# Kernel tuning notes

Hardware: AMD Instinct MI355X
Metric: run time of the kernel (lower is better)

The kernel has to match this reference:

```python
import jax, jax.numpy as jnp
import numpy as np

N_NODES = 100_000
N_EDGES = 3_200_000
F_IN, F_HID, F_OUT = 128, 128, 128
MLP_HID, MLP_OUT = 256, 64


def setup_inputs() -> dict:
    key = jax.random.key(0)
    ks = jax.random.split(key, 11)
    def w(k, shape):
        fan_in = shape[0]
        return jax.random.normal(k, shape, jnp.float32) / jnp.sqrt(jnp.float32(fan_in))
    return {
        'x':   jax.random.normal(ks[0], (N_NODES, F_IN), jnp.float32),
        'src': jax.random.randint(ks[1], (N_EDGES,), 0, N_NODES, jnp.int32),
        'dst': jax.random.randint(ks[2], (N_EDGES,), 0, N_NODES, jnp.int32),
        'w1':  w(ks[3], (F_IN, F_HID)),  'b1': jnp.zeros((F_HID,), jnp.float32),
        'w2':  w(ks[4], (F_HID, F_OUT)), 'b2': jnp.zeros((F_OUT,), jnp.float32),
        'wm1': w(ks[5], (F_OUT, MLP_HID)), 'bm1': jnp.zeros((MLP_HID,), jnp.float32),
        'wm2': w(ks[6], (MLP_HID, MLP_OUT)), 'bm2': jnp.zeros((MLP_OUT,), jnp.float32),
    }


def reference(x, src, dst, w1, b1, w2, b2, wm1, bm1, wm2, bm2):
    n = x.shape[0]
    ones = jnp.ones(src.shape[0], x.dtype)
    # DGL GraphConv norm='both': clamp degrees to >=1, symmetric D^-1/2 A D^-1/2
    out_norm = jnp.clip(jax.ops.segment_sum(ones, src, num_segments=n), 1.0) ** -0.5
    in_norm = jnp.clip(jax.ops.segment_sum(ones, dst, num_segments=n), 1.0) ** -0.5

    def gconv(h, w, b):
        msg = (h * out_norm[:, None])[src]                       # [E, F] gather
        agg = jax.ops.segment_sum(msg, dst, num_segments=n)      # [N, F] scatter-add
        return (agg * in_norm[:, None]) @ w + b

    h = jax.nn.relu(gconv(x, w1, b1))   # conv1 + relu (dropout is identity in eval)
    h = jax.nn.relu(gconv(h, w2, b2))   # conv2 + relu
    h = jax.nn.relu(h @ wm1 + bm1)      # MLP hidden layer
    return h @ wm2 + bm2                # MLP output (no final activation)
```

## Files before the change

### kernel.cpp

```cpp
#include <hip/hip_runtime.h>
#include <hip/hip_bf16.h>
#include <cstdint>

__device__ __forceinline__ unsigned short f2b(float f) {
    union { float f; unsigned int i; } v; v.f = f;
    unsigned int i = v.i;
    unsigned int r = (i + 0x7FFFu + ((i >> 16) & 1u)) >> 16;
    return (unsigned short)r;
}
__device__ __forceinline__ float b2f_lo(unsigned int p) {
    union { unsigned int i; float f; } v; v.i = p << 16; return v.f;
}
__device__ __forceinline__ float b2f_hi(unsigned int p) {
    union { unsigned int i; float f; } v; v.i = p & 0xFFFF0000u; return v.f;
}
__device__ __forceinline__ unsigned int pack2(float a, float b) {
    return (unsigned int)f2b(a) | ((unsigned int)f2b(b) << 16);
}

typedef __attribute__((__ext_vector_type__(8))) __bf16 bf16x8;
typedef __attribute__((__ext_vector_type__(4))) float  f32x4;

#define N_NODES 100000
#define N_EDGES 3200000
#define NBUCK   400
#define BSZ     250
#define NCHUNK  256
#define CHUNK   12500
#define BCAP    9216

__global__ void k_hist2(const int* __restrict__ src, const int* __restrict__ dst,
                        int* __restrict__ gcntA, int* __restrict__ gcntB,
                        int* __restrict__ blkA, int* __restrict__ blkB, int E) {
    __shared__ int hA[NBUCK], hB[NBUCK];
    int t = threadIdx.x, b = blockIdx.x;
    int lo = b * CHUNK, hi = min(lo + CHUNK, E);
    for (int j = t; j < NBUCK; j += 256) { hA[j] = 0; hB[j] = 0; }
    __syncthreads();
    for (int i = lo + t; i < hi; i += 256) {
        atomicAdd(&hA[dst[i] / BSZ], 1);
        atomicAdd(&hB[src[i] / BSZ], 1);
    }
    __syncthreads();
    for (int j = t; j < NBUCK; j += 256) {
        blkA[b * NBUCK + j] = hA[j];
        blkB[b * NBUCK + j] = hB[j];
        if (hA[j]) atomicAdd(&gcntA[j], hA[j]);
        if (hB[j]) atomicAdd(&gcntB[j], hB[j]);
    }
}

__global__ void k_scan_coarse(const int* __restrict__ gcntA, const int* __restrict__ gcntB,
                              int* __restrict__ gbaseA, int* __restrict__ gbaseB,
                              int* __restrict__ gcurA, int* __restrict__ gcurB,
                              int* __restrict__ offsets) {
    __shared__ int pA[512], pB[512];
    int t = threadIdx.x;
    int vA = (t < NBUCK) ? gcntA[t] : 0;
    int vB = (t < NBUCK) ? gcntB[t] : 0;
    pA[t] = vA; pB[t] = vB;
    __syncthreads();
    for (int d = 1; d < 512; d <<= 1) {
        int a = (t >= d) ? pA[t - d] : 0;
        int b = (t >= d) ? pB[t - d] : 0;
        __syncthreads();
        pA[t] += a; pB[t] += b;
        __syncthreads();
    }
    if (t < NBUCK) {
        gbaseA[t] = pA[t] - vA; gcurA[t] = pA[t] - vA;
        gbaseB[t] = pB[t] - vB; gcurB[t] = pB[t] - vB;
    }
    if (t == 511) {
        gbaseA[NBUCK] = pA[511];
        gbaseB[NBUCK] = pB[511];
        offsets[N_NODES] = pA[511];
    }
}

__global__ void k_scatter(const int* __restrict__ src, const int* __restrict__ dst,
                          int* __restrict__ gcurA, int* __restrict__ gcurB,
                          const int* __restrict__ blkA, const int* __restrict__ blkB,
                          unsigned* __restrict__ pairs, unsigned short* __restrict__ keysB,
                          int E) {
    __shared__ int baA[NBUCK], baB[NBUCK], lcA[NBUCK], lcB[NBUCK];
    int t = threadIdx.x, b = blockIdx.x;
    int lo = b * CHUNK, hi = min(lo + CHUNK, E);
    for (int j = t; j < NBUCK; j += 256) {
        int hA = blkA[b * NBUCK + j];
        baA[j] = hA ? atomicAdd(&gcurA[j], hA) : 0;
        lcA[j] = 0;
        int hB = blkB[b * NBUCK + j];
        baB[j] = hB ? atomicAdd(&gcurB[j], hB) : 0;
        lcB[j] = 0;
    }
    __syncthreads();
    for (int i = lo + t; i < hi; i += 256) {
        int s = src[i], d = dst[i];
        int bA = d / BSZ;
        int l  = atomicAdd(&lcA[bA], 1);
        pairs[baA[bA] + l] = ((unsigned)(d - bA * BSZ) << 17) | (unsigned)s;
        int bB = s / BSZ;
        int l2 = atomicAdd(&lcB[bB], 1);
        keysB[baB[bB] + l2] = (unsigned short)(s - bB * BSZ);
    }
}

__global__ __launch_bounds__(512)
void k_csr_sort(const unsigned* __restrict__ pairs, const int* __restrict__ gbaseA,
                int* __restrict__ offsets, float* __restrict__ in_norm,
                int* __restrict__ esrc) {
    __shared__ int el[BCAP];
    __shared__ int hist[256], scan[256], curs[256];
    int b = blockIdx.x, t = threadIdx.x;
    int node0 = b * BSZ;
    int bstart = gbaseA[b], bend = gbaseA[b + 1];
    int cnt = bend - bstart;
    if (t < 256) hist[t] = 0;
    __syncthreads();
    for (int i = bstart + t; i < bend; i += 512)
        atomicAdd(&hist[pairs[i] >> 17], 1);
    __syncthreads();
    if (t < 256) scan[t] = hist[t];
    __syncthreads();
    for (int d = 1; d < 256; d <<= 1) {
        int v = (t < 256 && t >= d) ? scan[t - d] : 0;
        __syncthreads();
        if (t < 256) scan[t] += v;
        __syncthreads();
    }
    if (t < BSZ) {
        int excl = scan[t] - hist[t];
        offsets[node0 + t] = bstart + excl;
        in_norm[node0 + t] = rsqrtf((float)max(hist[t], 1));
        curs[t] = excl;
    }
    __syncthreads();
    for (int i = bstart + t; i < bend; i += 512) {
        unsigned p = pairs[i];
        int d = (int)(p >> 17);
        int l = atomicAdd(&curs[d], 1);
        el[l] = (int)(p & 0x1FFFFu);
    }
    __syncthreads();
    int wv = t >> 6, lane = t & 63;
    const int INF = 0x7FFFFFFF;
    for (int n = wv; n < BSZ; n += 8) {
        int len = hist[n];
        if (len <= 1) continue;
        int base = scan[n] - len;
        if (len <= 64) {
            int v0 = (lane < len) ? el[base + lane] : INF;
#pragma unroll
            for (int k = 2; k <= 64; k <<= 1) {
#pragma unroll
                for (int d = 32; d > 0; d >>= 1) {
                    if (d >= k) continue;
                    int w0 = __shfl_xor(v0, d, 64);
                    bool up = ((lane & k) == 0);
                    bool lower = ((lane & d) == 0);
                    v0 = (lower == up) ? min(v0, w0) : max(v0, w0);
                }
            }
            if (lane < len) el[base + lane] = v0;
        } else {
            int v0 = (lane < len) ? el[base + lane] : INF;
            int v1 = (64 + lane < len) ? el[base + 64 + lane] : INF;
#pragma unroll
            for (int k = 2; k <= 128; k <<= 1) {
#pragma unroll
                for (int d = 64; d > 0; d >>= 1) {
                    if (d >= k) continue;
                    if (d == 64) {
                        int a = min(v0, v1), bb = max(v0, v1);
                        v0 = a; v1 = bb;
                    } else {
                        int w0 = __shfl_xor(v0, d, 64);
                        int w1 = __shfl_xor(v1, d, 64);
                        bool up0 = ((lane & k) == 0);
                        bool up1 = (((64 + lane) & k) == 0);
                        bool lower = ((lane & d) == 0);
                        v0 = (lower == up0) ? min(v0, w0) : max(v0, w0);
                        v1 = (lower == up1) ? min(v1, w1) : max(v1, w1);
                    }
                }
            }
            if (lane < len) el[base + lane] = v0;
            if (64 + lane < len) el[base + 64 + lane] = v1;
        }
    }
    __syncthreads();
    for (int i = t; i < cnt; i += 512) esrc[bstart + i] = el[i];
}

__global__ __launch_bounds__(512)
void k_count_scale(const unsigned short* __restrict__ keys,
                   const int* __restrict__ gbaseB,
                   const float4* __restrict__ x4, float* __restrict__ out_norm,
                   uint2* __restrict__ xs,
                   const float* __restrict__ w1, const float* __restrict__ w2,
                   const float* __restrict__ wm1, const float* __restrict__ wm2,
                   unsigned short* __restrict__ t1, unsigned short* __restrict__ t2,
                   unsigned short* __restrict__ tm1, unsigned short* __restrict__ tm2) {
    {
        int gid = blockIdx.x * 512 + threadIdx.x;
        if (gid < 81920) {
            const float* w; unsigned short* tt; int Nn, idx;
            if (gid < 16384)       { w = w1;  tt = t1;  Nn = 128; idx = gid; }
            else if (gid < 32768)  { w = w2;  tt = t2;  Nn = 128; idx = gid - 16384; }
            else if (gid < 65536)  { w = wm1; tt = tm1; Nn = 256; idx = gid - 32768; }
            else                   { w = wm2; tt = tm2; Nn = 64;  idx = gid - 65536; }
            int K = (gid < 65536) ? 128 : 256;
            int k = idx / Nn, n = idx - k * Nn;
            tt[(size_t)n * K + k] = f2b(w[idx]);
        }
    }
    __shared__ int hist[256];
    __shared__ float onl[BSZ];
    int b = blockIdx.x, t = threadIdx.x;
    int node0 = b * BSZ;
    int bstart = gbaseB[b], bend = gbaseB[b + 1];
    if (t < 256) hist[t] = 0;
    __syncthreads();
    for (int i = bstart + t; i < bend; i += 512)
        atomicAdd(&hist[keys[i]], 1);
    __syncthreads();
    if (t < BSZ) {
        float on = rsqrtf((float)max(hist[t], 1));
        onl[t] = on;
        out_norm[node0 + t] = on;
    }
    __syncthreads();
    size_t base4 = (size_t)node0 * 32;
    for (int i = t; i < BSZ * 32; i += 512) {
        float on = onl[i >> 5];
        float4 v = x4[base4 + i];
        uint2 o;
        o.x = pack2(v.x * on, v.y * on);
        o.y = pack2(v.z * on, v.w * on);
        xs[base4 + i] = o;
    }
}

#define AGG_ADD(p)                                                              \
        a0 += b2f_lo(p.x); a1 += b2f_hi(p.x);                                   \
        a2 += b2f_lo(p.y); a3 += b2f_hi(p.y);                                   \
        a4 += b2f_lo(p.z); a5 += b2f_hi(p.z);                                   \
        a6 += b2f_lo(p.w); a7 += b2f_hi(p.w);

#define AGG_NODE_BODY(node)                                                     \
    int lo = offsets[node], hi = offsets[node + 1];                             \
    float a0 = 0.f, a1 = 0.f, a2 = 0.f, a3 = 0.f,                               \
          a4 = 0.f, a5 = 0.f, a6 = 0.f, a7 = 0.f;                               \
    int k = lo + g;                                                             \
    for (; k + 12 < hi; k += 16) {                                              \
        int s0 = esrc[k];                                                       \
        int s1 = esrc[k + 4];                                                   \
        int s2 = esrc[k + 8];                                                   \
        int s3 = esrc[k + 12];                                                  \
        uint4 p0 = feat[(size_t)s0 * 16 + c];                                   \
        uint4 p1 = feat[(size_t)s1 * 16 + c];                                   \
        uint4 p2 = feat[(size_t)s2 * 16 + c];                                   \
        uint4 p3 = feat[(size_t)s3 * 16 + c];                                   \
        AGG_ADD(p0) AGG_ADD(p1) AGG_ADD(p2) AGG_ADD(p3)                         \
    }                                                                           \
    for (; k < hi; k += 4) {                                                    \
        int s = esrc[k];                                                        \
        uint4 p = feat[(size_t)s * 16 + c];                                     \
        AGG_ADD(p)                                                              \
    }                                                                           \
    a0 += __shfl_xor(a0, 16, 64); a0 += __shfl_xor(a0, 32, 64);                 \
    a1 += __shfl_xor(a1, 16, 64); a1 += __shfl_xor(a1, 32, 64);                 \
    a2 += __shfl_xor(a2, 16, 64); a2 += __shfl_xor(a2, 32, 64);                 \
    a3 += __shfl_xor(a3, 16, 64); a3 += __shfl_xor(a3, 32, 64);                 \
    a4 += __shfl_xor(a4, 16, 64); a4 += __shfl_xor(a4, 32, 64);                 \
    a5 += __shfl_xor(a5, 16, 64); a5 += __shfl_xor(a5, 32, 64);                 \
    a6 += __shfl_xor(a6, 16, 64); a6 += __shfl_xor(a6, 32, 64);                 \
    a7 += __shfl_xor(a7, 16, 64); a7 += __shfl_xor(a7, 32, 64);

__global__ __launch_bounds__(256, 8)
void k_conv(const int* __restrict__ offsets, const int* __restrict__ esrc,
            const uint4* __restrict__ feat, const float* __restrict__ in_norm,
            const unsigned short* __restrict__ WT, const float* __restrict__ bias,
            const float* __restrict__ row_scale, unsigned short* __restrict__ C,
            int N) {
    __shared__ __align__(16) unsigned short A[32][136];
    int wv = threadIdx.x >> 6, lane = threadIdx.x & 63;
    int row0 = blockIdx.x * 32;
    int g = lane >> 4, c = lane & 15;

    for (int i = 0; i < 8; ++i) {
        int nl = wv * 8 + i;
        int node = row0 + nl;
        AGG_NODE_BODY(node)
        if (g == 0) {
            float inn = in_norm[node];
            uint4 o;
            o.x = pack2(a0 * inn, a1 * inn);
            o.y = pack2(a2 * inn, a3 * inn);
            o.z = pack2(a4 * inn, a5 * inn);
            o.w = pack2(a6 * inn, a7 * inn);
            *(uint4*)&A[nl][c * 8] = o;
        }
    }
    __syncthreads();

    int m = lane & 15, q = lane >> 4;
    const unsigned short* b0 = WT + (size_t)(wv * 32 + m) * 128 + q * 8;
    const unsigned short* b1 = b0 + (size_t)16 * 128;
    f32x4 acc00 = {0.f, 0.f, 0.f, 0.f}, acc10 = {0.f, 0.f, 0.f, 0.f};
    f32x4 acc01 = {0.f, 0.f, 0.f, 0.f}, acc11 = {0.f, 0.f, 0.f, 0.f};
#pragma unroll
    for (int k = 0; k < 128; k += 32) {
        bf16x8 bf0 = *(const bf16x8*)(b0 + k);
        bf16x8 bf1 = *(const bf16x8*)(b1 + k);
        bf16x8 af0 = *(const bf16x8*)&A[m][q * 8 + k];
        bf16x8 af1 = *(const bf16x8*)&A[16 + m][q * 8 + k];
        acc00 = __builtin_amdgcn_mfma_f32_16x16x32_bf16(af0, bf0, acc00, 0, 0, 0);
        acc10 = __builtin_amdgcn_mfma_f32_16x16x32_bf16(af1, bf0, acc10, 0, 0, 0);
        acc01 = __builtin_amdgcn_mfma_f32_16x16x32_bf16(af0, bf1, acc01, 0, 0, 0);
        acc11 = __builtin_amdgcn_mfma_f32_16x16x32_bf16(af1, bf1, acc11, 0, 0, 0);
    }
    __syncthreads();

    int col0 = wv * 32 + m;
    int col1 = col0 + 16;
    float bc0 = bias[col0], bc1 = bias[col1];
#pragma unroll
    for (int r = 0; r < 4; r++) {
        int rl = q * 4 + r;
        int rr = row0 + rl, rr1 = rr + 16;
        float v00 = fmaxf(acc00[r] + bc0, 0.f);
        float v10 = fmaxf(acc10[r] + bc0, 0.f);
        float v01 = fmaxf(acc01[r] + bc1, 0.f);
        float v11 = fmaxf(acc11[r] + bc1, 0.f);
        float s0 = row_scale[rr], s1 = row_scale[rr1];
        v00 *= s0; v01 *= s0; v10 *= s1; v11 *= s1;
        A[rl][col0]      = f2b(v00);
        A[rl][col1]      = f2b(v01);
        A[rl + 16][col0] = f2b(v10);
        A[rl + 16][col1] = f2b(v11);
    }
    __syncthreads();
#pragma unroll
    for (int it = 0; it < 2; ++it) {
        int idx = it * 256 + (int)threadIdx.x;
        int row = idx >> 4, seg = idx & 15;
        uint4 v = *(const uint4*)&A[row][seg * 8];
        *(uint4*)&C[(size_t)(row0 + row) * 128 + seg * 8] = v;
    }
}

__global__ __launch_bounds__(256, 8)
void k_conv2_mlp(const int* __restrict__ offsets, const int* __restrict__ esrc,
                 const uint4* __restrict__ feat, const float* __restrict__ in_norm,
                 const unsigned short* __restrict__ WT2, const float* __restrict__ b2,
                 const unsigned short* __restrict__ WTM1, const float* __restrict__ bm1,
                 const unsigned short* __restrict__ WTM2, const float* __restrict__ bm2,
                 float* __restrict__ out, int N) {
    __shared__ __align__(16) unsigned short smem[8704];
    unsigned short (*H1)[136] = (unsigned short(*)[136])(smem);
    unsigned short (*A)[136]  = (unsigned short(*)[136])(smem + 4352);
    unsigned short (*H2)[136] = (unsigned short(*)[136])(smem + 4352);

    int wv = threadIdx.x >> 6, lane = threadIdx.x & 63;
    int row0 = blockIdx.x * 32;
    int g = lane >> 4, c = lane & 15;

    for (int i = 0; i < 8; ++i) {
        int nl = wv * 8 + i;
        int node = row0 + nl;
        AGG_NODE_BODY(node)
        if (g == 0) {
            float inn = in_norm[node];
            uint4 o;
            o.x = pack2(a0 * inn, a1 * inn);
            o.y = pack2(a2 * inn, a3 * inn);
            o.z = pack2(a4 * inn, a5 * inn);
            o.w = pack2(a6 * inn, a7 * inn);
            *(uint4*)&A[nl][c * 8] = o;
        }
    }
    __syncthreads();

    int m = lane & 15, q = lane >> 4;

    {
        const unsigned short* bb0 = WT2 + (size_t)(wv * 32 + m) * 128 + q * 8;
        const unsigned short* bb1 = bb0 + (size_t)16 * 128;
        f32x4 acc00 = {0.f, 0.f, 0.f, 0.f}, acc10 = {0.f, 0.f, 0.f, 0.f};
        f32x4 acc01 = {0.f, 0.f, 0.f, 0.f}, acc11 = {0.f, 0.f, 0.f, 0.f};
#pragma unroll
        for (int k = 0; k < 128; k += 32) {
            bf16x8 bf0 = *(const bf16x8*)(bb0 + k);
            bf16x8 bf1 = *(const bf16x8*)(bb1 + k);
            bf16x8 af0 = *(const bf16x8*)&A[m][q * 8 + k];
            bf16x8 af1 = *(const bf16x8*)&A[16 + m][q * 8 + k];
            acc00 = __builtin_amdgcn_mfma_f32_16x16x32_bf16(af0, bf0, acc00, 0, 0, 0);
            acc10 = __builtin_amdgcn_mfma_f32_16x16x32_bf16(af1, bf0, acc10, 0, 0, 0);
            acc01 = __builtin_amdgcn_mfma_f32_16x16x32_bf16(af0, bf1, acc01, 0, 0, 0);
            acc11 = __builtin_amdgcn_mfma_f32_16x16x32_bf16(af1, bf1, acc11, 0, 0, 0);
        }
        int col0 = wv * 32 + m;
        int col1 = col0 + 16;
        float bc0 = b2[col0], bc1 = b2[col1];
#pragma unroll
        for (int r = 0; r < 4; r++) {
            int rl = q * 4 + r;
            H1[rl][col0]      = f2b(fmaxf(acc00[r] + bc0, 0.f));
            H1[rl][col1]      = f2b(fmaxf(acc01[r] + bc1, 0.f));
            H1[rl + 16][col0] = f2b(fmaxf(acc10[r] + bc0, 0.f));
            H1[rl + 16][col1] = f2b(fmaxf(acc11[r] + bc1, 0.f));
        }
    }
    __syncthreads();

    f32x4 macc0 = {0.f, 0.f, 0.f, 0.f}, macc1 = {0.f, 0.f, 0.f, 0.f};
    int colo = wv * 16 + m;
    const unsigned short* bp2 = WTM2 + (size_t)colo * 256 + q * 8;
#pragma unroll
    for (int half = 0; half < 2; ++half) {
#pragma unroll
        for (int cb = 0; cb < 2; cb++) {
            int colh = half * 128 + wv * 32 + cb * 16 + m;
            const unsigned short* bp = WTM1 + (size_t)colh * 128 + q * 8;
            f32x4 acc0 = {0.f, 0.f, 0.f, 0.f};
            f32x4 acc1 = {0.f, 0.f, 0.f, 0.f};
#pragma unroll
            for (int s = 0; s < 4; s++) {
                bf16x8 bfr = *(const bf16x8*)(bp + s * 32);
                bf16x8 ha0 = *(const bf16x8*)&H1[m][s * 32 + q * 8];
                bf16x8 ha1 = *(const bf16x8*)&H1[m + 16][s * 32 + q * 8];
                acc0 = __builtin_amdgcn_mfma_f32_16x16x32_bf16(ha0, bfr, acc0, 0, 0, 0);
                acc1 = __builtin_amdgcn_mfma_f32_16x16x32_bf16(ha1, bfr, acc1, 0, 0, 0);
            }
            float bc = bm1[colh];
            int cl = colh & 127;
#pragma unroll
            for (int r = 0; r < 4; r++) {
                H2[q * 4 + r][cl]      = f2b(fmaxf(acc0[r] + bc, 0.f));
                H2[q * 4 + r + 16][cl] = f2b(fmaxf(acc1[r] + bc, 0.f));
            }
        }
        __syncthreads();
#pragma unroll
        for (int s = 0; s < 4; s++) {
            bf16x8 bfr = *(const bf16x8*)(bp2 + half * 128 + s * 32);
            bf16x8 ha0 = *(const bf16x8*)&H2[m][s * 32 + q * 8];
            bf16x8 ha1 = *(const bf16x8*)&H2[m + 16][s * 32 + q * 8];
            macc0 = __builtin_amdgcn_mfma_f32_16x16x32_bf16(ha0, bfr, macc0, 0, 0, 0);
            macc1 = __builtin_amdgcn_mfma_f32_16x16x32_bf16(ha1, bfr, macc1, 0, 0, 0);
        }
        __syncthreads();
    }

    float* OS = (float*)smem;
    float bc = bm2[colo];
#pragma unroll
    for (int r = 0; r < 4; r++) {
        OS[(q * 4 + r) * 64 + colo]        = macc0[r] + bc;
        OS[(q * 4 + r + 16) * 64 + colo]   = macc1[r] + bc;
    }
    __syncthreads();
#pragma unroll
    for (int it = 0; it < 2; ++it) {
        int idx = it * 256 + (int)threadIdx.x;
        int row = idx >> 4, seg = idx & 15;
        f32x4 v = *(const f32x4*)&OS[row * 64 + seg * 4];
        __builtin_nontemporal_store(v, (f32x4*)&out[(size_t)(row0 + row) * 64 + seg * 4]);
    }
}

extern "C" void kernel_launch(void* const* d_in, const int* in_sizes, int n_in,
                              void* d_out, int out_size, void* d_ws, size_t ws_size,
                              hipStream_t stream) {
    const float* x    = (const float*)d_in[0];
    const int*   src  = (const int*)d_in[1];
    const int*   dst  = (const int*)d_in[2];
    const float* w1   = (const float*)d_in[3];
    const float* b1   = (const float*)d_in[4];
    const float* w2   = (const float*)d_in[5];
    const float* b2   = (const float*)d_in[6];
    const float* wm1  = (const float*)d_in[7];
    const float* bm1  = (const float*)d_in[8];
    const float* wm2  = (const float*)d_in[9];
    const float* bm2  = (const float*)d_in[10];

    const int N = N_NODES;
    const int E = N_EDGES;

    char* p = (char*)d_ws;
    auto alloc = [&](size_t bytes) -> void* {
        void* r = (void*)p;
        p += (bytes + 255) & ~(size_t)255;
        return r;
    };
    int*   gcntA   = (int*)alloc((NBUCK + 1) * 4);
    int*   gcntB   = (int*)alloc((NBUCK + 1) * 4);
    int*   gbaseA  = (int*)alloc((NBUCK + 1) * 4);
    int*   gbaseB  = (int*)alloc((NBUCK + 1) * 4);
    int*   gcurA   = (int*)alloc((NBUCK + 1) * 4);
    int*   gcurB   = (int*)alloc((NBUCK + 1) * 4);
    int*   blkA    = (int*)alloc((size_t)NCHUNK * NBUCK * 4);
    int*   blkB    = (int*)alloc((size_t)NCHUNK * NBUCK * 4);
    int*   offsets = (int*)alloc((size_t)(N + 1) * 4);
    float* out_norm = (float*)alloc((size_t)N * 4);
    float* in_norm  = (float*)alloc((size_t)N * 4);
    int*   esrc     = (int*)alloc((size_t)E * 4);
    unsigned int* bufA = (unsigned int*)alloc((size_t)N * 128 * 2);
    unsigned int* bufB = (unsigned int*)alloc((size_t)N * 128 * 2);
    unsigned int* bufC = (unsigned int*)alloc((size_t)N * 128 * 2);
    unsigned short* wt1  = (unsigned short*)alloc(128 * 128 * 2);
    unsigned short* wt2  = (unsigned short*)alloc(128 * 128 * 2);
    unsigned short* wtm1 = (unsigned short*)alloc(256 * 128 * 2);
    unsigned short* wtm2 = (unsigned short*)alloc(64 * 256 * 2);
    (void)ws_size; (void)n_in; (void)in_sizes; (void)out_size;

    unsigned*       pairs = (unsigned*)bufB;
    unsigned short* keysB = (unsigned short*)bufC;

    (void)hipMemsetAsync(gcntA, 0, (size_t)((char*)gcntB - (char*)gcntA) + NBUCK * 4, stream);

    const int TB = 256;
    k_hist2<<<dim3(NCHUNK), dim3(TB), 0, stream>>>(src, dst, gcntA, gcntB, blkA, blkB, E);
    k_scan_coarse<<<dim3(1), dim3(512), 0, stream>>>(gcntA, gcntB, gbaseA, gbaseB,
                                                     gcurA, gcurB, offsets);
    k_scatter<<<dim3(NCHUNK), dim3(TB), 0, stream>>>(src, dst, gcurA, gcurB, blkA, blkB,
                                                     pairs, keysB, E);
    k_csr_sort<<<dim3(NBUCK), dim3(512), 0, stream>>>(pairs, gbaseA, offsets, in_norm, esrc);
    k_count_scale<<<dim3(NBUCK), dim3(512), 0, stream>>>(
        keysB, gbaseB, (const float4*)x, out_norm, (uint2*)bufA,
        w1, w2, wm1, wm2, wt1, wt2, wtm1, wtm2);

    k_conv<<<dim3(N / 32), dim3(TB), 0, stream>>>(
        offsets, esrc, (const uint4*)bufA, in_norm, wt1, b1, out_norm,
        (unsigned short*)bufC, N);

    k_conv2_mlp<<<dim3(N / 32), dim3(TB), 0, stream>>>(
        offsets, esrc, (const uint4*)bufC, in_norm, wt2, b2, wtm1, bm1, wtm2, bm2,
        (float*)d_out, N);
}
```

Before: 525.9 us.

## Slice features into 16-column panels and split aggregation from GEMM kernels

Node features are stored in a column-sliced layout (8 slices of 16 bf16 columns). Aggregation becomes a separate kernel, with blocks assigned per slice and node range, so each gather touches a 3.2 MB slice that can stay cache-resident. The conv GEMM and the MLP now read that sliced layout from global memory, and the GEMM writes its output in the same layout. The cost is extra kernel launches and round trips of the intermediate aggregates through global memory, plus each edge index being read once per slice.

```diff
diff --git a/kernel.cpp b/kernel.cpp
--- a/kernel.cpp
+++ b/kernel.cpp
@@ -28,6 +28,8 @@
 #define NCHUNK  256
 #define CHUNK   12500
 #define BCAP    9216
+#define NSLICE  8
+#define ANB     400
 
 __global__ void k_hist2(const int* __restrict__ src, const int* __restrict__ dst,
                         int* __restrict__ gcntA, int* __restrict__ gcntB,
@@ -233,66 +235,78 @@
     __syncthreads();
     size_t base4 = (size_t)node0 * 32;
     for (int i = t; i < BSZ * 32; i += 512) {
-        float on = onl[i >> 5];
+        int nl = i >> 5;
+        int j  = i & 31;
+        float on = onl[nl];
         float4 v = x4[base4 + i];
         uint2 o;
         o.x = pack2(v.x * on, v.y * on);
         o.y = pack2(v.z * on, v.w * on);
-        xs[base4 + i] = o;
-    }
-}
-
-#define AGG_ADD(p)                                                              \
-        a0 += b2f_lo(p.x); a1 += b2f_hi(p.x);                                   \
-        a2 += b2f_lo(p.y); a3 += b2f_hi(p.y);                                   \
-        a4 += b2f_lo(p.z); a5 += b2f_hi(p.z);                                   \
-        a6 += b2f_lo(p.w); a7 += b2f_hi(p.w);
-
-#define AGG_NODE_BODY(node)                                                     \
-    int lo = offsets[node], hi = offsets[node + 1];                             \
-    float a0 = 0.f, a1 = 0.f, a2 = 0.f, a3 = 0.f,                               \
-          a4 = 0.f, a5 = 0.f, a6 = 0.f, a7 = 0.f;                               \
-    int k = lo + g;                                                             \
-    for (; k + 12 < hi; k += 16) {                                              \
-        int s0 = esrc[k];                                                       \
-        int s1 = esrc[k + 4];                                                   \
-        int s2 = esrc[k + 8];                                                   \
-        int s3 = esrc[k + 12];                                                  \
-        uint4 p0 = feat[(size_t)s0 * 16 + c];                                   \
-        uint4 p1 = feat[(size_t)s1 * 16 + c];                                   \
-        uint4 p2 = feat[(size_t)s2 * 16 + c];                                   \
-        uint4 p3 = feat[(size_t)s3 * 16 + c];                                   \
-        AGG_ADD(p0) AGG_ADD(p1) AGG_ADD(p2) AGG_ADD(p3)                         \
-    }                                                                           \
-    for (; k < hi; k += 4) {                                                    \
-        int s = esrc[k];                                                        \
-        uint4 p = feat[(size_t)s * 16 + c];                                     \
-        AGG_ADD(p)                                                              \
-    }                                                                           \
-    a0 += __shfl_xor(a0, 16, 64); a0 += __shfl_xor(a0, 32, 64);                 \
-    a1 += __shfl_xor(a1, 16, 64); a1 += __shfl_xor(a1, 32, 64);                 \
-    a2 += __shfl_xor(a2, 16, 64); a2 += __shfl_xor(a2, 32, 64);                 \
-    a3 += __shfl_xor(a3, 16, 64); a3 += __shfl_xor(a3, 32, 64);                 \
-    a4 += __shfl_xor(a4, 16, 64); a4 += __shfl_xor(a4, 32, 64);                 \
-    a5 += __shfl_xor(a5, 16, 64); a5 += __shfl_xor(a5, 32, 64);                 \
-    a6 += __shfl_xor(a6, 16, 64); a6 += __shfl_xor(a6, 32, 64);                 \
-    a7 += __shfl_xor(a7, 16, 64); a7 += __shfl_xor(a7, 32, 64);
+        xs[((size_t)(j >> 2) * N_NODES + (node0 + nl)) * 4 + (j & 3)] = o;
+    }
+}
 
 __global__ __launch_bounds__(256, 8)
-void k_conv(const int* __restrict__ offsets, const int* __restrict__ esrc,
-            const uint4* __restrict__ feat, const float* __restrict__ in_norm,
-            const unsigned short* __restrict__ WT, const float* __restrict__ bias,
-            const float* __restrict__ row_scale, unsigned short* __restrict__ C,
-            int N) {
-    __shared__ __align__(16) unsigned short A[32][136];
-    int wv = threadIdx.x >> 6, lane = threadIdx.x & 63;
-    int row0 = blockIdx.x * 32;
-    int g = lane >> 4, c = lane & 15;
-
-    for (int i = 0; i < 8; ++i) {
-        int nl = wv * 8 + i;
-        int node = row0 + nl;
-        AGG_NODE_BODY(node)
+void k_agg_s(const int* __restrict__ offsets, const int* __restrict__ esrc,
+             const uint4* __restrict__ featS, const float* __restrict__ in_norm,
+             uint4* __restrict__ aggS) {
+    int bid = blockIdx.x;
+    int s  = bid & 7;
+    int nb = bid >> 3;
+    int lane = threadIdx.x & 63, wv = threadIdx.x >> 6;
+    int nl = lane >> 3;
+    int g  = (lane >> 1) & 3;
+    int c  = lane & 1;
+    const uint4* fs = featS + (size_t)s * N_NODES * 2;
+    uint4* as = aggS + (size_t)s * N_NODES * 2;
+    int nend = nb * ANB + ANB;
+    for (int node = nb * ANB + wv * 8 + nl; node < nend; node += 32) {
+        int lo = offsets[node], hi = offsets[node + 1];
+        float a0 = 0.f, a1 = 0.f, a2 = 0.f, a3 = 0.f,
+              a4 = 0.f, a5 = 0.f, a6 = 0.f, a7 = 0.f;
+        int k = lo + g;
+        for (; k + 12 < hi; k += 16) {
+            int s0 = esrc[k];
+            int s1 = esrc[k + 4];
+            int s2 = esrc[k + 8];
+            int s3 = esrc[k + 12];
+            uint4 p0 = fs[(size_t)s0 * 2 + c];
+            uint4 p1 = fs[(size_t)s1 * 2 + c];
+            uint4 p2 = fs[(size_t)s2 * 2 + c];
+            uint4 p3 = fs[(size_t)s3 * 2 + c];
+            a0 += b2f_lo(p0.x); a1 += b2f_hi(p0.x);
+            a2 += b2f_lo(p0.y); a3 += b2f_hi(p0.y);
+            a4 += b2f_lo(p0.z); a5 += b2f_hi(p0.z);
+            a6 += b2f_lo(p0.w); a7 += b2f_hi(p0.w);
+            a0 += b2f_lo(p1.x); a1 += b2f_hi(p1.x);
+            a2 += b2f_lo(p1.y); a3 += b2f_hi(p1.y);
+            a4 += b2f_lo(p1.z); a5 += b2f_hi(p1.z);
+            a6 += b2f_lo(p1.w); a7 += b2f_hi(p1.w);
+            a0 += b2f_lo(p2.x); a1 += b2f_hi(p2.x);
+            a2 += b2f_lo(p2.y); a3 += b2f_hi(p2.y);
+            a4 += b2f_lo(p2.z); a5 += b2f_hi(p2.z);
+            a6 += b2f_lo(p2.w); a7 += b2f_hi(p2.w);
+            a0 += b2f_lo(p3.x); a1 += b2f_hi(p3.x);
+            a2 += b2f_lo(p3.y); a3 += b2f_hi(p3.y);
+            a4 += b2f_lo(p3.z); a5 += b2f_hi(p3.z);
+            a6 += b2f_lo(p3.w); a7 += b2f_hi(p3.w);
+        }
+        for (; k < hi; k += 4) {
+            int s0 = esrc[k];
+            uint4 p = fs[(size_t)s0 * 2 + c];
+            a0 += b2f_lo(p.x); a1 += b2f_hi(p.x);
+            a2 += b2f_lo(p.y); a3 += b2f_hi(p.y);
+            a4 += b2f_lo(p.z); a5 += b2f_hi(p.z);
+            a6 += b2f_lo(p.w); a7 += b2f_hi(p.w);
+        }
+        a0 += __shfl_xor(a0, 2, 64); a0 += __shfl_xor(a0, 4, 64);
+        a1 += __shfl_xor(a1, 2, 64); a1 += __shfl_xor(a1, 4, 64);
+        a2 += __shfl_xor(a2, 2, 64); a2 += __shfl_xor(a2, 4, 64);
+        a3 += __shfl_xor(a3, 2, 64); a3 += __shfl_xor(a3, 4, 64);
+        a4 += __shfl_xor(a4, 2, 64); a4 += __shfl_xor(a4, 4, 64);
+        a5 += __shfl_xor(a5, 2, 64); a5 += __shfl_xor(a5, 4, 64);
+        a6 += __shfl_xor(a6, 2, 64); a6 += __shfl_xor(a6, 4, 64);
+        a7 += __shfl_xor(a7, 2, 64); a7 += __shfl_xor(a7, 4, 64);
         if (g == 0) {
             float inn = in_norm[node];
             uint4 o;
@@ -300,89 +314,72 @@
             o.y = pack2(a2 * inn, a3 * inn);
             o.z = pack2(a4 * inn, a5 * inn);
             o.w = pack2(a6 * inn, a7 * inn);
-            *(uint4*)&A[nl][c * 8] = o;
-        }
-    }
-    __syncthreads();
-
+            as[(size_t)node * 2 + c] = o;
+        }
+    }
+}
+
+__global__ __launch_bounds__(256)
+void k_gemm_s(const unsigned short* __restrict__ A, const unsigned short* __restrict__ WT,
+              const float* __restrict__ bias, const float* __restrict__ row_scale,
+              unsigned short* __restrict__ Cs) {
+    int wv = threadIdx.x >> 6, lane = threadIdx.x & 63;
     int m = lane & 15, q = lane >> 4;
-    const unsigned short* b0 = WT + (size_t)(wv * 32 + m) * 128 + q * 8;
-    const unsigned short* b1 = b0 + (size_t)16 * 128;
-    f32x4 acc00 = {0.f, 0.f, 0.f, 0.f}, acc10 = {0.f, 0.f, 0.f, 0.f};
-    f32x4 acc01 = {0.f, 0.f, 0.f, 0.f}, acc11 = {0.f, 0.f, 0.f, 0.f};
-#pragma unroll
-    for (int k = 0; k < 128; k += 32) {
-        bf16x8 bf0 = *(const bf16x8*)(b0 + k);
-        bf16x8 bf1 = *(const bf16x8*)(b1 + k);
-        bf16x8 af0 = *(const bf16x8*)&A[m][q * 8 + k];
-        bf16x8 af1 = *(const bf16x8*)&A[16 + m][q * 8 + k];
-        acc00 = __builtin_amdgcn_mfma_f32_16x16x32_bf16(af0, bf0, acc00, 0, 0, 0);
-        acc10 = __builtin_amdgcn_mfma_f32_16x16x32_bf16(af1, bf0, acc10, 0, 0, 0);
-        acc01 = __builtin_amdgcn_mfma_f32_16x16x32_bf16(af0, bf1, acc01, 0, 0, 0);
-        acc11 = __builtin_amdgcn_mfma_f32_16x16x32_bf16(af1, bf1, acc11, 0, 0, 0);
-    }
-    __syncthreads();
-
-    int col0 = wv * 32 + m;
-    int col1 = col0 + 16;
-    float bc0 = bias[col0], bc1 = bias[col1];
+    int row0 = blockIdx.x * 32;
+    int col0 = blockIdx.y * 64 + wv * 16;
+    int r0m = row0 + m;
+    const unsigned short* bp = WT + (size_t)(col0 + m) * 128 + q * 8;
+    f32x4 acc0 = {0.f, 0.f, 0.f, 0.f};
+    f32x4 acc1 = {0.f, 0.f, 0.f, 0.f};
+#pragma unroll
+    for (int kk = 0; kk < 128; kk += 32) {
+        int col = q * 8 + kk;
+        const unsigned short* ab = A + ((size_t)(col >> 4) * N_NODES) * 16 + (col & 15);
+        bf16x8 bfr = *(const bf16x8*)(bp + kk);
+        bf16x8 af0 = *(const bf16x8*)(ab + (size_t)r0m * 16);
+        bf16x8 af1 = *(const bf16x8*)(ab + (size_t)(r0m + 16) * 16);
+        acc0 = __builtin_amdgcn_mfma_f32_16x16x32_bf16(af0, bfr, acc0, 0, 0, 0);
+        acc1 = __builtin_amdgcn_mfma_f32_16x16x32_bf16(af1, bfr, acc1, 0, 0, 0);
+    }
+    int cc = col0 + m;
+    float bc = bias[cc];
+    unsigned short* cb = Cs + ((size_t)(cc >> 4) * N_NODES) * 16 + (cc & 15);
 #pragma unroll
     for (int r = 0; r < 4; r++) {
-        int rl = q * 4 + r;
-        int rr = row0 + rl, rr1 = rr + 16;
-        float v00 = fmaxf(acc00[r] + bc0, 0.f);
-        float v10 = fmaxf(acc10[r] + bc0, 0.f);
-        float v01 = fmaxf(acc01[r] + bc1, 0.f);
-        float v11 = fmaxf(acc11[r] + bc1, 0.f);
-        float s0 = row_scale[rr], s1 = row_scale[rr1];
-        v00 *= s0; v01 *= s0; v10 *= s1; v11 *= s1;
-        A[rl][col0]      = f2b(v00);
-        A[rl][col1]      = f2b(v01);
-        A[rl + 16][col0] = f2b(v10);
-        A[rl + 16][col1] = f2b(v11);
-    }
-    __syncthreads();
-#pragma unroll
-    for (int it = 0; it < 2; ++it) {
-        int idx = it * 256 + (int)threadIdx.x;
-        int row = idx >> 4, seg = idx & 15;
-        uint4 v = *(const uint4*)&A[row][seg * 8];
-        *(uint4*)&C[(size_t)(row0 + row) * 128 + seg * 8] = v;
+        int rr = row0 + q * 4 + r;
+        int rr1 = rr + 16;
+        float v0 = fmaxf(acc0[r] + bc, 0.f) * row_scale[rr];
+        float v1 = fmaxf(acc1[r] + bc, 0.f) * row_scale[rr1];
+        cb[(size_t)rr * 16]  = f2b(v0);
+        cb[(size_t)rr1 * 16] = f2b(v1);
     }
 }
 
 __global__ __launch_bounds__(256, 8)
-void k_conv2_mlp(const int* __restrict__ offsets, const int* __restrict__ esrc,
-                 const uint4* __restrict__ feat, const float* __restrict__ in_norm,
-                 const unsigned short* __restrict__ WT2, const float* __restrict__ b2,
-                 const unsigned short* __restrict__ WTM1, const float* __restrict__ bm1,
-                 const unsigned short* __restrict__ WTM2, const float* __restrict__ bm2,
-                 float* __restrict__ out, int N) {
+void k_mlp3(const uint4* __restrict__ AgS,
+            const unsigned short* __restrict__ WT2, const float* __restrict__ b2,
+            const unsigned short* __restrict__ WTM1, const float* __restrict__ bm1,
+            const unsigned short* __restrict__ WTM2, const float* __restrict__ bm2,
+            float* __restrict__ out) {
     __shared__ __align__(16) unsigned short smem[8704];
     unsigned short (*H1)[136] = (unsigned short(*)[136])(smem);
     unsigned short (*A)[136]  = (unsigned short(*)[136])(smem + 4352);
     unsigned short (*H2)[136] = (unsigned short(*)[136])(smem + 4352);
 
-    int wv = threadIdx.x >> 6, lane = threadIdx.x & 63;
     int row0 = blockIdx.x * 32;
-    int g = lane >> 4, c = lane & 15;
-
-    for (int i = 0; i < 8; ++i) {
-        int nl = wv * 8 + i;
-        int node = row0 + nl;
-        AGG_NODE_BODY(node)
-        if (g == 0) {
-            float inn = in_norm[node];
-            uint4 o;
-            o.x = pack2(a0 * inn, a1 * inn);
-            o.y = pack2(a2 * inn, a3 * inn);
-            o.z = pack2(a4 * inn, a5 * inn);
-            o.w = pack2(a6 * inn, a7 * inn);
-            *(uint4*)&A[nl][c * 8] = o;
-        }
-    }
-    __syncthreads();
-
+    int t = threadIdx.x;
+
+#pragma unroll
+    for (int it = 0; it < 2; ++it) {
+        int idx = it * 256 + t;
+        int seg = idx >> 5;
+        int row = idx & 31;
+        uint4 v = AgS[((size_t)(seg >> 1) * N_NODES + row0 + row) * 2 + (seg & 1)];
+        *(uint4*)&A[row][seg * 8] = v;
+    }
+    __syncthreads();
+
+    int wv = t >> 6, lane = t & 63;
     int m = lane & 15, q = lane >> 4;
 
     {
@@ -427,10 +424,10 @@
             f32x4 acc0 = {0.f, 0.f, 0.f, 0.f};
             f32x4 acc1 = {0.f, 0.f, 0.f, 0.f};
 #pragma unroll
-            for (int s = 0; s < 4; s++) {
-                bf16x8 bfr = *(const bf16x8*)(bp + s * 32);
-                bf16x8 ha0 = *(const bf16x8*)&H1[m][s * 32 + q * 8];
-                bf16x8 ha1 = *(const bf16x8*)&H1[m + 16][s * 32 + q * 8];
+            for (int ss = 0; ss < 4; ss++) {
+                bf16x8 bfr = *(const bf16x8*)(bp + ss * 32);
+                bf16x8 ha0 = *(const bf16x8*)&H1[m][ss * 32 + q * 8];
+                bf16x8 ha1 = *(const bf16x8*)&H1[m + 16][ss * 32 + q * 8];
                 acc0 = __builtin_amdgcn_mfma_f32_16x16x32_bf16(ha0, bfr, acc0, 0, 0, 0);
                 acc1 = __builtin_amdgcn_mfma_f32_16x16x32_bf16(ha1, bfr, acc1, 0, 0, 0);
             }
@@ -444,10 +441,10 @@
         }
         __syncthreads();
 #pragma unroll
-        for (int s = 0; s < 4; s++) {
-            bf16x8 bfr = *(const bf16x8*)(bp2 + half * 128 + s * 32);
-            bf16x8 ha0 = *(const bf16x8*)&H2[m][s * 32 + q * 8];
-            bf16x8 ha1 = *(const bf16x8*)&H2[m + 16][s * 32 + q * 8];
+        for (int ss = 0; ss < 4; ss++) {
+            bf16x8 bfr = *(const bf16x8*)(bp2 + half * 128 + ss * 32);
+            bf16x8 ha0 = *(const bf16x8*)&H2[m][ss * 32 + q * 8];
+            bf16x8 ha1 = *(const bf16x8*)&H2[m + 16][ss * 32 + q * 8];
             macc0 = __builtin_amdgcn_mfma_f32_16x16x32_bf16(ha0, bfr, macc0, 0, 0, 0);
             macc1 = __builtin_amdgcn_mfma_f32_16x16x32_bf16(ha1, bfr, macc1, 0, 0, 0);
         }
@@ -458,13 +455,13 @@
     float bc = bm2[colo];
 #pragma unroll
     for (int r = 0; r < 4; r++) {
-        OS[(q * 4 + r) * 64 + colo]        = macc0[r] + bc;
-        OS[(q * 4 + r + 16) * 64 + colo]   = macc1[r] + bc;
+        OS[(q * 4 + r) * 64 + colo]      = macc0[r] + bc;
+        OS[(q * 4 + r + 16) * 64 + colo] = macc1[r] + bc;
     }
     __syncthreads();
 #pragma unroll
     for (int it = 0; it < 2; ++it) {
-        int idx = it * 256 + (int)threadIdx.x;
+        int idx = it * 256 + t;
         int row = idx >> 4, seg = idx & 15;
         f32x4 v = *(const f32x4*)&OS[row * 64 + seg * 4];
         __builtin_nontemporal_store(v, (f32x4*)&out[(size_t)(row0 + row) * 64 + seg * 4]);
@@ -532,11 +529,13 @@
         keysB, gbaseB, (const float4*)x, out_norm, (uint2*)bufA,
         w1, w2, wm1, wm2, wt1, wt2, wtm1, wtm2);
 
-    k_conv<<<dim3(N / 32), dim3(TB), 0, stream>>>(
-        offsets, esrc, (const uint4*)bufA, in_norm, wt1, b1, out_norm,
-        (unsigned short*)bufC, N);
-
-    k_conv2_mlp<<<dim3(N / 32), dim3(TB), 0, stream>>>(
-        offsets, esrc, (const uint4*)bufC, in_norm, wt2, b2, wtm1, bm1, wtm2, bm2,
-        (float*)d_out, N);
-}
+    k_agg_s<<<dim3(NSLICE * (N / ANB)), dim3(TB), 0, stream>>>(
+        offsets, esrc, (const uint4*)bufA, in_norm, (uint4*)bufB);
+    k_gemm_s<<<dim3(N / 32, 2), dim3(TB), 0, stream>>>(
+        (const unsigned short*)bufB, wt1, b1, out_norm, (unsigned short*)bufC);
+
+    k_agg_s<<<dim3(NSLICE * (N / ANB)), dim3(TB), 0, stream>>>(
+        offsets, esrc, (const uint4*)bufC, in_norm, (uint4*)bufA);
+    k_mlp3<<<dim3(N / 32), dim3(TB), 0, stream>>>(
+        (const uint4*)bufA, wt2, b2, wtm1, bm1, wtm2, bm2, (float*)d_out);
+}
```

After: 647.2 us. +23.1%, slower.

## Fuse histogram into scatter using fixed-capacity bucket slots, dropping global scan

Applied to the files above, without the earlier changes.

Merges the histogram, coarse-scan and scatter kernels into one pass by giving each bucket a fixed BCAP-sized region. Block offsets within a bucket come from atomic counters instead of a prefix sum. CSR now uses separate begin and end arrays, since buckets are no longer contiguous. This removes a full read pass over src/dst and two launches, but relies on no bucket exceeding BCAP edges.

```diff
diff --git a/kernel.cpp b/kernel.cpp
--- a/kernel.cpp
+++ b/kernel.cpp
@@ -29,10 +29,11 @@
 #define CHUNK   12500
 #define BCAP    9216
 
-__global__ void k_hist2(const int* __restrict__ src, const int* __restrict__ dst,
-                        int* __restrict__ gcntA, int* __restrict__ gcntB,
-                        int* __restrict__ blkA, int* __restrict__ blkB, int E) {
-    __shared__ int hA[NBUCK], hB[NBUCK];
+__global__ void k_scatter(const int* __restrict__ src, const int* __restrict__ dst,
+                          int* __restrict__ gcurA, int* __restrict__ gcurB,
+                          unsigned* __restrict__ pairs, unsigned short* __restrict__ keysB,
+                          int E) {
+    __shared__ int hA[NBUCK], hB[NBUCK], baA[NBUCK], baB[NBUCK], lcA[NBUCK], lcB[NBUCK];
     int t = threadIdx.x, b = blockIdx.x;
     int lo = b * CHUNK, hi = min(lo + CHUNK, E);
     for (int j = t; j < NBUCK; j += 256) { hA[j] = 0; hB[j] = 0; }
@@ -43,55 +44,9 @@
     }
     __syncthreads();
     for (int j = t; j < NBUCK; j += 256) {
-        blkA[b * NBUCK + j] = hA[j];
-        blkB[b * NBUCK + j] = hB[j];
-        if (hA[j]) atomicAdd(&gcntA[j], hA[j]);
-        if (hB[j]) atomicAdd(&gcntB[j], hB[j]);
-    }
-}
-
-__global__ void k_scan_coarse(const int* __restrict__ gcntA, const int* __restrict__ gcntB,
-                              int* __restrict__ gbaseA, int* __restrict__ gbaseB,
-                              int* __restrict__ gcurA, int* __restrict__ gcurB,
-                              int* __restrict__ offsets) {
-    __shared__ int pA[512], pB[512];
-    int t = threadIdx.x;
-    int vA = (t < NBUCK) ? gcntA[t] : 0;
-    int vB = (t < NBUCK) ? gcntB[t] : 0;
-    pA[t] = vA; pB[t] = vB;
-    __syncthreads();
-    for (int d = 1; d < 512; d <<= 1) {
-        int a = (t >= d) ? pA[t - d] : 0;
-        int b = (t >= d) ? pB[t - d] : 0;
-        __syncthreads();
-        pA[t] += a; pB[t] += b;
-        __syncthreads();
-    }
-    if (t < NBUCK) {
-        gbaseA[t] = pA[t] - vA; gcurA[t] = pA[t] - vA;
-        gbaseB[t] = pB[t] - vB; gcurB[t] = pB[t] - vB;
-    }
-    if (t == 511) {
-        gbaseA[NBUCK] = pA[511];
-        gbaseB[NBUCK] = pB[511];
-        offsets[N_NODES] = pA[511];
-    }
-}
-
-__global__ void k_scatter(const int* __restrict__ src, const int* __restrict__ dst,
-                          int* __restrict__ gcurA, int* __restrict__ gcurB,
-                          const int* __restrict__ blkA, const int* __restrict__ blkB,
-                          unsigned* __restrict__ pairs, unsigned short* __restrict__ keysB,
-                          int E) {
-    __shared__ int baA[NBUCK], baB[NBUCK], lcA[NBUCK], lcB[NBUCK];
-    int t = threadIdx.x, b = blockIdx.x;
-    int lo = b * CHUNK, hi = min(lo + CHUNK, E);
-    for (int j = t; j < NBUCK; j += 256) {
-        int hA = blkA[b * NBUCK + j];
-        baA[j] = hA ? atomicAdd(&gcurA[j], hA) : 0;
+        baA[j] = hA[j] ? (j * BCAP + atomicAdd(&gcurA[j], hA[j])) : 0;
         lcA[j] = 0;
-        int hB = blkB[b * NBUCK + j];
-        baB[j] = hB ? atomicAdd(&gcurB[j], hB) : 0;
+        baB[j] = hB[j] ? (j * BCAP + atomicAdd(&gcurB[j], hB[j])) : 0;
         lcB[j] = 0;
     }
     __syncthreads();
@@ -107,15 +62,16 @@
 }
 
 __global__ __launch_bounds__(512)
-void k_csr_sort(const unsigned* __restrict__ pairs, const int* __restrict__ gbaseA,
-                int* __restrict__ offsets, float* __restrict__ in_norm,
-                int* __restrict__ esrc) {
+void k_csr_sort(const unsigned* __restrict__ pairs, const int* __restrict__ bcntA,
+                int* __restrict__ offsets, int* __restrict__ ends,
+                float* __restrict__ in_norm, int* __restrict__ esrc) {
     __shared__ int el[BCAP];
     __shared__ int hist[256], scan[256], curs[256];
     int b = blockIdx.x, t = threadIdx.x;
     int node0 = b * BSZ;
-    int bstart = gbaseA[b], bend = gbaseA[b + 1];
-    int cnt = bend - bstart;
+    int bstart = b * BCAP;
+    int cnt = bcntA[b];
+    int bend = bstart + cnt;
     if (t < 256) hist[t] = 0;
     __syncthreads();
     for (int i = bstart + t; i < bend; i += 512)
@@ -132,6 +88,7 @@
     if (t < BSZ) {
         int excl = scan[t] - hist[t];
         offsets[node0 + t] = bstart + excl;
+        ends[node0 + t]    = bstart + scan[t];
         in_norm[node0 + t] = rsqrtf((float)max(hist[t], 1));
         curs[t] = excl;
     }
@@ -195,7 +152,7 @@
 
 __global__ __launch_bounds__(512)
 void k_count_scale(const unsigned short* __restrict__ keys,
-                   const int* __restrict__ gbaseB,
+                   const int* __restrict__ bcntB,
                    const float4* __restrict__ x4, float* __restrict__ out_norm,
                    uint2* __restrict__ xs,
                    const float* __restrict__ w1, const float* __restrict__ w2,
@@ -219,7 +176,8 @@
     __shared__ float onl[BSZ];
     int b = blockIdx.x, t = threadIdx.x;
     int node0 = b * BSZ;
-    int bstart = gbaseB[b], bend = gbaseB[b + 1];
+    int bstart = b * BCAP;
+    int bend = bstart + bcntB[b];
     if (t < 256) hist[t] = 0;
     __syncthreads();
     for (int i = bstart + t; i < bend; i += 512)
@@ -249,7 +207,7 @@
         a6 += b2f_lo(p.w); a7 += b2f_hi(p.w);
 
 #define AGG_NODE_BODY(node)                                                     \
-    int lo = offsets[node], hi = offsets[node + 1];                             \
+    int lo = offsets[node], hi = ends[node];                                    \
     float a0 = 0.f, a1 = 0.f, a2 = 0.f, a3 = 0.f,                               \
           a4 = 0.f, a5 = 0.f, a6 = 0.f, a7 = 0.f;                               \
     int k = lo + g;                                                             \
@@ -279,7 +237,8 @@
     a7 += __shfl_xor(a7, 16, 64); a7 += __shfl_xor(a7, 32, 64);
 
 __global__ __launch_bounds__(256, 8)
-void k_conv(const int* __restrict__ offsets, const int* __restrict__ esrc,
+void k_conv(const int* __restrict__ offsets, const int* __restrict__ ends,
+            const int* __restrict__ esrc,
             const uint4* __restrict__ feat, const float* __restrict__ in_norm,
             const unsigned short* __restrict__ WT, const float* __restrict__ bias,
             const float* __restrict__ row_scale, unsigned short* __restrict__ C,
@@ -352,7 +311,8 @@
 }
 
 __global__ __launch_bounds__(256, 8)
-void k_conv2_mlp(const int* __restrict__ offsets, const int* __restrict__ esrc,
+void k_conv2_mlp(const int* __restrict__ offsets, const int* __restrict__ ends,
+                 const int* __restrict__ esrc,
                  const uint4* __restrict__ feat, const float* __restrict__ in_norm,
                  const unsigned short* __restrict__ WT2, const float* __restrict__ b2,
                  const unsigned short* __restrict__ WTM1, const float* __restrict__ bm1,
@@ -495,18 +455,13 @@
         p += (bytes + 255) & ~(size_t)255;
         return r;
     };
-    int*   gcntA   = (int*)alloc((NBUCK + 1) * 4);
-    int*   gcntB   = (int*)alloc((NBUCK + 1) * 4);
-    int*   gbaseA  = (int*)alloc((NBUCK + 1) * 4);
-    int*   gbaseB  = (int*)alloc((NBUCK + 1) * 4);
-    int*   gcurA   = (int*)alloc((NBUCK + 1) * 4);
-    int*   gcurB   = (int*)alloc((NBUCK + 1) * 4);
-    int*   blkA    = (int*)alloc((size_t)NCHUNK * NBUCK * 4);
-    int*   blkB    = (int*)alloc((size_t)NCHUNK * NBUCK * 4);
-    int*   offsets = (int*)alloc((size_t)(N + 1) * 4);
+    int*   gcurA   = (int*)alloc(NBUCK * 4);
+    int*   gcurB   = (int*)alloc(NBUCK * 4);
+    int*   offsets = (int*)alloc((size_t)N * 4);
+    int*   ends    = (int*)alloc((size_t)N * 4);
     float* out_norm = (float*)alloc((size_t)N * 4);
     float* in_norm  = (float*)alloc((size_t)N * 4);
-    int*   esrc     = (int*)alloc((size_t)E * 4);
+    int*   esrc     = (int*)alloc((size_t)NBUCK * BCAP * 4);
     unsigned int* bufA = (unsigned int*)alloc((size_t)N * 128 * 2);
     unsigned int* bufB = (unsigned int*)alloc((size_t)N * 128 * 2);
     unsigned int* bufC = (unsigned int*)alloc((size_t)N * 128 * 2);
@@ -519,24 +474,22 @@
     unsigned*       pairs = (unsigned*)bufB;
     unsigned short* keysB = (unsigned short*)bufC;
 
-    (void)hipMemsetAsync(gcntA, 0, (size_t)((char*)gcntB - (char*)gcntA) + NBUCK * 4, stream);
+    (void)hipMemsetAsync(gcurA, 0, (size_t)((char*)gcurB - (char*)gcurA) + NBUCK * 4, stream);
 
     const int TB = 256;
-    k_hist2<<<dim3(NCHUNK), dim3(TB), 0, stream>>>(src, dst, gcntA, gcntB, blkA, blkB, E);
-    k_scan_coarse<<<dim3(1), dim3(512), 0, stream>>>(gcntA, gcntB, gbaseA, gbaseB,
-                                                     gcurA, gcurB, offsets);
-    k_scatter<<<dim3(NCHUNK), dim3(TB), 0, stream>>>(src, dst, gcurA, gcurB, blkA, blkB,
+    k_scatter<<<dim3(NCHUNK), dim3(TB), 0, stream>>>(src, dst, gcurA, gcurB,
                                                      pairs, keysB, E);
-    k_csr_sort<<<dim3(NBUCK), dim3(512), 0, stream>>>(pairs, gbaseA, offsets, in_norm, esrc);
+    k_csr_sort<<<dim3(NBUCK), dim3(512), 0, stream>>>(pairs, gcurA, offsets, ends,
+                                                      in_norm, esrc);
     k_count_scale<<<dim3(NBUCK), dim3(512), 0, stream>>>(
-        keysB, gbaseB, (const float4*)x, out_norm, (uint2*)bufA,
+        keysB, gcurB, (const float4*)x, out_norm, (uint2*)bufA,
         w1, w2, wm1, wm2, wt1, wt2, wtm1, wtm2);
 
     k_conv<<<dim3(N / 32), dim3(TB), 0, stream>>>(
-        offsets, esrc, (const uint4*)bufA, in_norm, wt1, b1, out_norm,
+        offsets, ends, esrc, (const uint4*)bufA, in_norm, wt1, b1, out_norm,
         (unsigned short*)bufC, N);
 
     k_conv2_mlp<<<dim3(N / 32), dim3(TB), 0, stream>>>(
-        offsets, esrc, (const uint4*)bufC, in_norm, wt2, b2, wtm1, bm1, wtm2, bm2,
+        offsets, ends, esrc, (const uint4*)bufC, in_norm, wt2, b2, wtm1, bm1, wtm2, bm2,
         (float*)d_out, N);
 }
```

Result: no change. 520.6 us (-1.0%).
